# Kernel optimization log

Hardware: AMD Instinct MI355X
Metric: run time of the kernel (lower is better)

The kernel has to match this reference:

```python
import jax, jax.numpy as jnp
import numpy as np

# Config constants from the module
E = 64    # n_routed_experts
K = 6     # num_experts_per_tok
D = 128   # hidden_size
M = 80    # moe_intermediate_size
MS = 160  # shared expert intermediate = moe_intermediate_size * n_shared_experts
B, S = 64, 256

def _init_w(k, shape, fan_in):
    # kaiming_uniform(a=sqrt(5)) used by nn.Linear / MoEGate: bound = 1/sqrt(fan_in)
    bound = 1.0 / np.sqrt(fan_in)
    return jax.random.uniform(k, shape, jnp.float32, -bound, bound)

def setup_inputs() -> dict:
    key = jax.random.key(0)
    ks = jax.random.split(key, 8)
    return {
        "hidden_states": jax.random.normal(ks[0], (B, S, D), jnp.float32),
        "gate_w": _init_w(ks[1], (E, D), D),        # MoEGate.linear.weight [E, gating_dim]
        "wg": _init_w(ks[2], (E, D, M), D),          # stacked expert gate_proj (transposed)
        "wu": _init_w(ks[3], (E, D, M), D),          # stacked expert up_proj
        "wd": _init_w(ks[4], (E, M, D), M),          # stacked expert down_proj
        "swg": _init_w(ks[5], (D, MS), D),           # shared expert gate_proj
        "swu": _init_w(ks[6], (D, MS), D),           # shared expert up_proj
        "swd": _init_w(ks[7], (MS, D), MS),          # shared expert down_proj
    }

def reference(hidden_states, gate_w, wg, wu, wd, swg, swu, swd):
    orig_shape = hidden_states.shape
    x = hidden_states.reshape(-1, D)                       # [T, D] flat tokens
    T = x.shape[0]
    # --- MoEGate ('all_agent' mode): softmax scoring + top-k + renorm ---
    scores = jax.nn.softmax(x @ gate_w.T, axis=-1)          # [T, E]
    topk_w, topk_idx = jax.lax.top_k(scores, K)             # [T, K]
    topk_w = topk_w / (jnp.sum(topk_w, axis=-1, keepdims=True) + 1e-20)
    # Scatter top-k weights into dense per-expert combine weights [T, E]
    cw = jnp.zeros_like(scores).at[jnp.arange(T)[:, None], topk_idx].add(topk_w)
    # --- Routed experts: SiLU-gated MLP per expert, combined by cw ---
    g = jax.nn.silu(jnp.einsum('td,edm->tem', x, wg)) * jnp.einsum('td,edm->tem', x, wu)
    y = jnp.einsum('tem,emd,te->td', g, wd, cw)             # down-proj + weighted combine
    # --- Shared experts ---
    shared = (jax.nn.silu(x @ swg) * (x @ swu)) @ swd       # [T, D]
    return (y + shared).reshape(orig_shape)
```

## Files before the change

kernel.cpp:

```cpp
#include <hip/hip_runtime.h>
#include <hip/hip_bf16.h>
#include <math.h>


typedef unsigned short ushort_t;
typedef __attribute__((ext_vector_type(8))) short bf16x8;
typedef __attribute__((ext_vector_type(4))) float f32x4;

#define EALL  66

#define OFF_TOPKI 16384
#define OFF_WORK  409600
#define OFF_TOPKW 802816
#define OFF_PERM  1196032
#define OFF_PERMW 1589248
#define OFF_POS2  1982464
#define OFF_YPERM 2375680
#define OFF_YSH   27541504
#define OFF_WGT   31735808
#define OFF_WUT   33087488
#define OFF_WDP   34439168
#define OFF_XB    36061184
#define OFF_HIST  40255488
#define OFF_BOFF  40321024
#define NEED_FAST 40386560
#define FOFF_YBUF 2375680
#define FOFF_WGT  10764288
#define FOFF_WUT  12115968
#define FOFF_WDP  13467648
#define FOFF_XB   15089664
#define FOFF_HIST 19283968
#define FOFF_BOFF 19349504

__device__ __forceinline__ float bf2f(ushort_t u) {
    unsigned int x = ((unsigned int)u) << 16;
    float f; __builtin_memcpy(&f, &x, 4); return f;
}
__device__ __forceinline__ ushort_t f2bf(float f) {
    unsigned int x; __builtin_memcpy(&x, &f, 4);
    unsigned int r = (x + 0x7fffu + ((x >> 16) & 1u)) >> 16;
    return (ushort_t)r;
}
__device__ __forceinline__ float ldin(const void* p, int i, int f32m) {
    return f32m ? ((const float*)p)[i] : bf2f(((const ushort_t*)p)[i]);
}
__device__ __forceinline__ int detect_f32m(const ushort_t* gw) {
    int lane = threadIdx.x & 63;
    int cnt = 0;
    #pragma unroll
    for (int j = 0; j < 4; ++j) {
        ushort_t u = gw[lane * 4 + j];
        if (((u >> 7) & 0xFF) >= 0x7C) cnt++;
    }
    #pragma unroll
    for (int off = 32; off; off >>= 1) cnt += __shfl_xor(cnt, off);
    return (cnt >= 8) ? 1 : 0;
}
__device__ __forceinline__ void gl16(void* l, const void* g) {
    __builtin_amdgcn_global_load_lds(
        (const __attribute__((address_space(1))) void*)g,
        (__attribute__((address_space(3))) void*)l, 16, 0, 0);
}

__global__ __launch_bounds__(1024) void k_pg(const void* x, const void* gw,
        const void* wg, const void* wu, const void* wd,
        const void* swg, const void* swu, const void* swd,
        ushort_t* wgT, ushort_t* wuT, ushort_t* wdP,
        ushort_t* xB, int* topk_i, float* topk_w, int* histPart) {
    __shared__ __align__(16) char smem[41984];
    int tid = threadIdx.x, bid = blockIdx.x;
    int f32m = detect_f32m((const ushort_t*)gw);

    if (bid < 3 * EALL) {
        float* lds = (float*)smem;
        int mat = bid / EALL, e = bid % EALL;
        if (mat < 2) {
            const void* src  = (mat == 0) ? wg  : wu;
            const void* ssrc = (mat == 0) ? swg : swu;
            for (int i = tid; i < 10240; i += 1024) {
                int d = i / 80, m = i % 80;
                float v = (e < 64) ? ldin(src, e * 10240 + i, f32m)
                                   : ldin(ssrc, d * 160 + (e - 64) * 80 + m, f32m);
                lds[d * 81 + m] = v;
            }
            __syncthreads();
            ushort_t* dst = ((mat == 0) ? wgT : wuT) + e * 10240;
            for (int o = tid; o < 10240; o += 1024) {
                int m = o >> 7, d = o & 127;
                dst[o] = f2bf(lds[d * 81 + m]);
            }
        } else {
            for (int i = tid; i < 10240; i += 1024) {
                float v = (e < 64) ? ldin(wd, e * 10240 + i, f32m)
                                   : ldin(swd, (e - 64) * 10240 + i, f32m);
                int m = i >> 7, d = i & 127;
                lds[m * 129 + d] = v;
            }
            __syncthreads();
            ushort_t* dst = wdP + e * 12288;
            for (int o = tid; o < 12288; o += 1024) {
                int d = o / 96, m = o % 96;
                dst[o] = (m < 80) ? f2bf(lds[m * 129 + d]) : (ushort_t)0;
            }
        }
        return;
    }

    float* gwl  = (float*)smem;
    float (*xl)[128] = (float(*)[128])(smem + 33280);
    int*   histL = (int*)(smem + 41472);
    int b = bid - 3 * EALL;
    for (int i = tid; i < 8192; i += 1024)
        gwl[(i >> 7) * 130 + (i & 127)] = ldin(gw, i, f32m);
    if (tid < 64) histL[tid] = 0;
    __syncthreads();
    int wv = tid >> 6, lane = tid & 63;
    for (int q = 0; q < 4; ++q) {
        int t = b * 64 + wv * 4 + q;
        float xv0, xv1;
        if (f32m) {
            float2 v = ((const float2*)((const float*)x + t * 128))[lane];
            xv0 = v.x; xv1 = v.y;
        } else {
            unsigned int pr = *(const unsigned int*)((const ushort_t*)x + t * 128 + lane * 2);
            xv0 = bf2f((ushort_t)(pr & 0xffffu));
            xv1 = bf2f((ushort_t)(pr >> 16));
        }
        float2 xw; xw.x = xv0; xw.y = xv1;
        *(float2*)&xl[wv][lane * 2] = xw;
        unsigned int packed = (unsigned int)f2bf(xv0) | ((unsigned int)f2bf(xv1) << 16);
        *(unsigned int*)(xB + t * 128 + lane * 2) = packed;
        float acc = 0.f;
        #pragma unroll
        for (int d2 = 0; d2 < 64; ++d2) {
            float2 xv = *(const float2*)&xl[wv][d2 * 2];
            float2 gv = *(const float2*)&gwl[lane * 130 + d2 * 2];
            acc = fmaf(xv.x, gv.x, acc);
            acc = fmaf(xv.y, gv.y, acc);
        }
        float mx = acc;
        #pragma unroll
        for (int off = 32; off; off >>= 1) mx = fmaxf(mx, __shfl_xor(mx, off));
        float p = expf(acc - mx);
        float sm = p;
        #pragma unroll
        for (int off = 32; off; off >>= 1) sm += __shfl_xor(sm, off);
        float sc = p / sm;
        float cur = sc;
        float wk6[6]; int ik[6];
        #pragma unroll
        for (int k = 0; k < 6; ++k) {
            float bv = cur; int bi = lane;
            #pragma unroll
            for (int off = 1; off < 64; off <<= 1) {
                float ov = __shfl_xor(bv, off); int oi = __shfl_xor(bi, off);
                if (ov > bv || (ov == bv && oi < bi)) { bv = ov; bi = oi; }
            }
            wk6[k] = bv; ik[k] = bi;
            if (lane == bi) cur = -INFINITY;
        }
        if (lane == 0) {
            float den = wk6[0] + wk6[1] + wk6[2] + wk6[3] + wk6[4] + wk6[5] + 1e-20f;
            #pragma unroll
            for (int k = 0; k < 6; ++k) {
                topk_i[t * 6 + k] = ik[k];
                topk_w[t * 6 + k] = wk6[k] / den;
                atomicAdd(&histL[ik[k]], 1);
            }
        }
    }
    __syncthreads();
    if (tid < 64) histPart[tid * 256 + b] = histL[tid];
}

__global__ __launch_bounds__(256) void k_scan(int* Wi, const int* histPart,
        int* boffG, int* wk) {
    __shared__ int hl[16384];
    __shared__ int cntL[64], exclL[64], chxL[65];
    int tid = threadIdx.x, lane = tid & 63, wv = tid >> 6;
    for (int j = tid; j < 16384; j += 256) hl[j] = histPart[j];
    __syncthreads();
    for (int ei = 0; ei < 16; ++ei) {
        int e = wv * 16 + ei;
        int carry = 0;
        for (int r = 0; r < 4; ++r) {
            int v = hl[e * 256 + r * 64 + lane];
            int incl = v;
            #pragma unroll
            for (int off = 1; off < 64; off <<= 1) {
                int ts = __shfl_up(incl, off);
                if (lane >= off) incl += ts;
            }
            hl[e * 256 + r * 64 + lane] = carry + incl - v;
            carry += __shfl(incl, 63);
        }
        if (lane == 0) cntL[e] = carry;
    }
    __syncthreads();
    if (tid == 0) {
        int s = 0, cs = 0;
        for (int e = 0; e < 64; ++e) {
            exclL[e] = s; s += cntL[e];
            chxL[e] = cs; cs += (cntL[e] + 127) >> 7;
        }
        chxL[64] = cs;
        Wi[128] = s;
        Wi[193] = cs + 256;
    }
    __syncthreads();
    if (tid < 64) { Wi[tid] = cntL[tid]; Wi[64 + tid] = exclL[tid]; }
    for (int j = tid; j < 16384; j += 256) boffG[j] = hl[j] + exclL[j >> 8];
    wk[tid] = (64 << 16) | tid;
    if (tid < 64) {
        int e = tid, nc = (cntL[e] + 127) >> 7, bb = chxL[e];
        for (int c = 0; c < nc; ++c) wk[256 + bb + c] = (e << 16) | c;
    }
}

__global__ __launch_bounds__(256) void k_scatter(const int* topk_i, const float* topk_w,
        const int* boffG, int* perm, float* permw, int* pos2) {
    __shared__ int lcur[64];
    int tid = threadIdx.x, b = blockIdx.x;
    if (tid < 64) lcur[tid] = boffG[tid * 256 + b];
    __syncthreads();
    for (int i = tid; i < 384; i += 256) {
        int g = b * 384 + i;
        int e = topk_i[g];
        float w = topk_w[g];
        int p = atomicAdd(&lcur[e], 1);
        perm[p]  = b * 64 + i / 6;
        permw[p] = w;
        pos2[g]  = p;
    }
}

template<int FAST>
__global__ __launch_bounds__(256) void k_expert(const ushort_t* x, const ushort_t* wgT,
        const ushort_t* wuT, const ushort_t* wdP, const int* Wi, const int* wk,
        const int* perm, const float* permw, ushort_t* yperm, ushort_t* ysh, float* ybuf) {
    __shared__ __align__(16) char hl[32768];
    __shared__ __align__(16) char bufA[20480];
    __shared__ __align__(16) char bufB[20480];

    if (blockIdx.x >= Wi[193]) return;
    int entry = wk[blockIdx.x];
    int e = entry >> 16, c = entry & 0xffff;
    int tid = threadIdx.x, lid = tid & 63, wv = tid >> 6;
    int kg  = (lid >> 4) * 16;
    int kq8 = (lid >> 4) * 8;

    if (e < 64) {
        int n = Wi[e], base = Wi[64 + e];
        int nrows = n - c * 128; if (nrows > 128) nrows = 128;

        {
            const ushort_t* gS = wgT + e * 10240;
            const ushort_t* uS = wuT + e * 10240;
            #pragma unroll
            for (int i = 0; i < 5; ++i) {
                int s = wv * 320 + i * 64 + lid;
                int row = s >> 4, sc = (s & 15) ^ (row & 7);
                gl16(bufA + wv * 5120 + i * 1024, gS + row * 128 + sc * 8);
                gl16(bufB + wv * 5120 + i * 1024, uS + row * 128 + sc * 8);
            }
        }
        bf16x8 a[2][4];
        #pragma unroll
        for (int tr = 0; tr < 2; ++tr) {
            int arow = wv * 32 + tr * 16 + (lid & 15);
            int r = (arow < nrows) ? arow : (nrows - 1);
            int t = perm[base + c * 128 + r];
            #pragma unroll
            for (int k = 0; k < 4; ++k)
                a[tr][k] = *(const bf16x8*)(x + t * 128 + k * 32 + kq8);
        }
        __syncthreads();

        #pragma unroll
        for (int mi = 0; mi < 5; ++mi) {
            int brow = mi * 16 + (lid & 15);
            int bro = brow * 256, bsw = (brow & 7) << 4;
            f32x4 ag[2], au[2];
            #pragma unroll
            for (int tr = 0; tr < 2; ++tr) {
                ag[tr] = (f32x4){0.f, 0.f, 0.f, 0.f};
                au[tr] = (f32x4){0.f, 0.f, 0.f, 0.f};
            }
            #pragma unroll
            for (int k = 0; k < 4; ++k) {
                int bo = bro + (((k * 64) + kg) ^ bsw);
                bf16x8 bg = *(const bf16x8*)(bufA + bo);
                bf16x8 bu = *(const bf16x8*)(bufB + bo);
                #pragma unroll
                for (int tr = 0; tr < 2; ++tr) {
                    ag[tr] = __builtin_amdgcn_mfma_f32_16x16x32_bf16(a[tr][k], bg, ag[tr], 0, 0, 0);
                    au[tr] = __builtin_amdgcn_mfma_f32_16x16x32_bf16(a[tr][k], bu, au[tr], 0, 0, 0);
                }
            }
            #pragma unroll
            for (int tr = 0; tr < 2; ++tr) {
                #pragma unroll
                for (int rg = 0; rg < 4; ++rg) {
                    float g = ag[tr][rg], uu2 = au[tr][rg];
                    float h = (g / (1.f + __expf(-g))) * uu2;
                    int row = wv * 32 + tr * 16 + (lid >> 4) * 4 + rg;
                    int cb = (mi * 16 + (lid & 15)) * 2;
                    *(ushort_t*)(hl + row * 256 + (cb ^ ((row & 7) << 4))) = f2bf(h);
                }
            }
        }
        {
            int r = wv * 32 + (lid >> 1), ch = 10 + (lid & 1);
            uint4 z = {0u, 0u, 0u, 0u};
            *(uint4*)(hl + r * 256 + ((ch * 16) ^ ((r & 7) << 4))) = z;
        }
        __syncthreads();

        {
            const ushort_t* dS = wdP + e * 12288;
            #pragma unroll
            for (int i = 0; i < 4; ++i) {
                int s = wv * 256 + i * 64 + lid;
                int r = s >> 4, sc = (s & 15) ^ (r & 7);
                int off = (sc < 12) ? sc * 8 : 0;
                gl16(bufA + wv * 4096 + i * 1024, dS + r * 96 + off);
                gl16(bufB + wv * 4096 + i * 1024, dS + (64 + r) * 96 + off);
            }
        }
        __syncthreads();

        f32x4 acc[8][2];
        #pragma unroll
        for (int dt = 0; dt < 8; ++dt) {
            acc[dt][0] = (f32x4){0.f, 0.f, 0.f, 0.f};
            acc[dt][1] = (f32x4){0.f, 0.f, 0.f, 0.f};
        }
        #pragma unroll
        for (int dt = 0; dt < 8; ++dt) {
            int r = (dt & 3) * 16 + (lid & 15);
            const char* wb = (dt < 4) ? bufA : bufB;
            bf16x8 ad[3];
            #pragma unroll
            for (int k = 0; k < 3; ++k)
                ad[k] = *(const bf16x8*)(wb + r * 256 + (((k * 64) + kg) ^ ((r & 7) << 4)));
            #pragma unroll
            for (int tf = 0; tf < 2; ++tf) {
                int brow = wv * 32 + tf * 16 + (lid & 15);
                f32x4 cc = acc[dt][tf];
                #pragma unroll
                for (int k = 0; k < 3; ++k) {
                    bf16x8 b = *(const bf16x8*)(hl + brow * 256 + (((k * 64) + kg) ^ ((brow & 7) << 4)));
                    cc = __builtin_amdgcn_mfma_f32_16x16x32_bf16(ad[k], b, cc, 0, 0, 0);
                }
                acc[dt][tf] = cc;
            }
        }

        #pragma unroll
        for (int tf = 0; tf < 2; ++tf) {
            int rloc = wv * 32 + tf * 16 + (lid & 15);
            int rc = (rloc < nrows) ? rloc : (nrows - 1);
            float w = FAST ? permw[base + c * 128 + rc] : 0.f;
            #pragma unroll
            for (int dt = 0; dt < 8; ++dt) {
                if (FAST) {
                    int cb = (dt * 16 + (lid >> 4) * 4) * 2;
                    ushort_t o[4];
                    #pragma unroll
                    for (int rg = 0; rg < 4; ++rg) o[rg] = f2bf(acc[dt][tf][rg] * w);
                    *(uint2*)(hl + rloc * 256 + (cb ^ ((rloc & 7) << 4))) = *(const uint2*)o;
                } else {
                    if (rloc < nrows) {
                        int t = perm[base + c * 128 + rloc];
                        float w2 = permw[base + c * 128 + rloc];
                        int d0 = dt * 16 + (lid >> 4) * 4;
                        #pragma unroll
                        for (int rg = 0; rg < 4; ++rg)
                            atomicAdd(&ybuf[t * 128 + d0 + rg], acc[dt][tf][rg] * w2);
                    }
                }
            }
        }
        if (FAST) {
            #pragma unroll
            for (int ps = 0; ps < 8; ++ps) {
                int row = wv * 32 + ps * 4 + (lid >> 4);
                int cb = (lid & 15) * 16;
                uint4 v = *(const uint4*)(hl + row * 256 + (cb ^ ((row & 7) << 4)));
                if (row < nrows)
                    *(uint4*)(yperm + (size_t)(base + c * 128 + row) * 128 + (lid & 15) * 8) = v;
            }
        }
    } else {
        bf16x8 a1[4];
        int arow = wv * 16 + (lid & 15);
        int t0 = c * 64 + arow;
        #pragma unroll
        for (int k = 0; k < 4; ++k)
            a1[k] = *(const bf16x8*)(x + t0 * 128 + k * 32 + kq8);

        f32x4 acc[8];
        #pragma unroll
        for (int dt = 0; dt < 8; ++dt) acc[dt] = (f32x4){0.f, 0.f, 0.f, 0.f};

        for (int sub = 0; sub < 2; ++sub) {
            int ee = 64 + sub;
            {
                const ushort_t* gS = wgT + ee * 10240;
                const ushort_t* uS = wuT + ee * 10240;
                #pragma unroll
                for (int i = 0; i < 5; ++i) {
                    int s = wv * 320 + i * 64 + lid;
                    int row = s >> 4, sc = (s & 15) ^ (row & 7);
                    gl16(bufA + wv * 5120 + i * 1024, gS + row * 128 + sc * 8);
                    gl16(bufB + wv * 5120 + i * 1024, uS + row * 128 + sc * 8);
                }
            }
            __syncthreads();
            #pragma unroll
            for (int mi = 0; mi < 5; ++mi) {
                int brow = mi * 16 + (lid & 15);
                int bro = brow * 256, bsw = (brow & 7) << 4;
                f32x4 ag = {0.f, 0.f, 0.f, 0.f};
                f32x4 au = {0.f, 0.f, 0.f, 0.f};
                #pragma unroll
                for (int k = 0; k < 4; ++k) {
                    int bo = bro + (((k * 64) + kg) ^ bsw);
                    bf16x8 bg = *(const bf16x8*)(bufA + bo);
                    bf16x8 bu = *(const bf16x8*)(bufB + bo);
                    ag = __builtin_amdgcn_mfma_f32_16x16x32_bf16(a1[k], bg, ag, 0, 0, 0);
                    au = __builtin_amdgcn_mfma_f32_16x16x32_bf16(a1[k], bu, au, 0, 0, 0);
                }
                #pragma unroll
                for (int rg = 0; rg < 4; ++rg) {
                    float g = ag[rg], uu2 = au[rg];
                    float h = (g / (1.f + __expf(-g))) * uu2;
                    int row = wv * 16 + (lid >> 4) * 4 + rg;
                    int cb = (mi * 16 + (lid & 15)) * 2;
                    *(ushort_t*)(hl + row * 256 + (cb ^ ((row & 7) << 4))) = f2bf(h);
                }
            }
            if (sub == 0 && lid < 32) {
                int r = wv * 16 + (lid >> 1), ch = 10 + (lid & 1);
                uint4 z = {0u, 0u, 0u, 0u};
                *(uint4*)(hl + r * 256 + ((ch * 16) ^ ((r & 7) << 4))) = z;
            }
            __syncthreads();
            {
                const ushort_t* dS = wdP + ee * 12288;
                #pragma unroll
                for (int i = 0; i < 4; ++i) {
                    int s = wv * 256 + i * 64 + lid;
                    int r = s >> 4, sc = (s & 15) ^ (r & 7);
                    int off = (sc < 12) ? sc * 8 : 0;
                    gl16(bufA + wv * 4096 + i * 1024, dS + r * 96 + off);
                    gl16(bufB + wv * 4096 + i * 1024, dS + (64 + r) * 96 + off);
                }
            }
            __syncthreads();
            int brow = wv * 16 + (lid & 15);
            #pragma unroll
            for (int dt = 0; dt < 8; ++dt) {
                int r = (dt & 3) * 16 + (lid & 15);
                const char* wb = (dt < 4) ? bufA : bufB;
                bf16x8 ad[3];
                #pragma unroll
                for (int k = 0; k < 3; ++k)
                    ad[k] = *(const bf16x8*)(wb + r * 256 + (((k * 64) + kg) ^ ((r & 7) << 4)));
                f32x4 cc = acc[dt];
                #pragma unroll
                for (int k = 0; k < 3; ++k) {
                    bf16x8 b = *(const bf16x8*)(hl + brow * 256 + (((k * 64) + kg) ^ ((brow & 7) << 4)));
                    cc = __builtin_amdgcn_mfma_f32_16x16x32_bf16(ad[k], b, cc, 0, 0, 0);
                }
                acc[dt] = cc;
            }
            __syncthreads();
        }

        int rloc = wv * 16 + (lid & 15);
        if (FAST) {
            #pragma unroll
            for (int dt = 0; dt < 8; ++dt) {
                int cb = (dt * 16 + (lid >> 4) * 4) * 2;
                ushort_t o[4];
                #pragma unroll
                for (int rg = 0; rg < 4; ++rg) o[rg] = f2bf(acc[dt][rg]);
                *(uint2*)(hl + rloc * 256 + (cb ^ ((rloc & 7) << 4))) = *(const uint2*)o;
            }
            #pragma unroll
            for (int ps = 0; ps < 4; ++ps) {
                int row = wv * 16 + ps * 4 + (lid >> 4);
                int cb = (lid & 15) * 16;
                uint4 v = *(const uint4*)(hl + row * 256 + (cb ^ ((row & 7) << 4)));
                *(uint4*)(ysh + (size_t)(c * 64 + row) * 128 + (lid & 15) * 8) = v;
            }
        } else {
            int t = c * 64 + rloc;
            #pragma unroll
            for (int dt = 0; dt < 8; ++dt) {
                int d0 = dt * 16 + (lid >> 4) * 4;
                #pragma unroll
                for (int rg = 0; rg < 4; ++rg)
                    atomicAdd(&ybuf[t * 128 + d0 + rg], acc[dt][rg]);
            }
        }
    }
}

__global__ __launch_bounds__(256) void k_final_gather(const ushort_t* yperm,
        const ushort_t* ysh, const int* pos2, void* out, const ushort_t* gwDet) {
    int idx = blockIdx.x * 256 + threadIdx.x;
    int t = idx >> 4, cg = (idx & 15) * 8;
    int f32m = detect_f32m(gwDet);
    float acc[8];
    {
        uint4 v = *(const uint4*)(ysh + (size_t)t * 128 + cg);
        const ushort_t* u = (const ushort_t*)&v;
        #pragma unroll
        for (int j = 0; j < 8; ++j) acc[j] = bf2f(u[j]);
    }
    const int* pp = pos2 + t * 6;
    #pragma unroll
    for (int k = 0; k < 6; ++k) {
        int p = pp[k];
        uint4 v = *(const uint4*)(yperm + (size_t)p * 128 + cg);
        const ushort_t* u = (const ushort_t*)&v;
        #pragma unroll
        for (int j = 0; j < 8; ++j) acc[j] += bf2f(u[j]);
    }
    if (f32m) {
        float4 o0 = {acc[0], acc[1], acc[2], acc[3]};
        float4 o1 = {acc[4], acc[5], acc[6], acc[7]};
        float* op = (float*)out + (size_t)t * 128 + cg;
        *(float4*)op = o0; *(float4*)(op + 4) = o1;
    } else {
        ushort_t o[8];
        #pragma unroll
        for (int j = 0; j < 8; ++j) o[j] = f2bf(acc[j]);
        *(uint4*)((ushort_t*)out + (size_t)t * 128 + cg) = *(const uint4*)o;
    }
}

__global__ __launch_bounds__(256) void k_final_ybuf(const float* ybuf, void* out,
        const ushort_t* gwDet) {
    int i = blockIdx.x * 256 + threadIdx.x;
    int f32m = detect_f32m(gwDet);
    float4 v = ((const float4*)ybuf)[i];
    if (f32m) {
        ((float4*)out)[i] = v;
    } else {
        ushort4 o;
        o.x = f2bf(v.x); o.y = f2bf(v.y); o.z = f2bf(v.z); o.w = f2bf(v.w);
        ((ushort4*)out)[i] = o;
    }
}

extern "C" void kernel_launch(void* const* d_in, const int* in_sizes, int n_in,
                              void* d_out, int out_size, void* d_ws, size_t ws_size,
                              hipStream_t stream) {
    (void)in_sizes; (void)n_in; (void)out_size;
    const void* x   = d_in[0];
    const void* gw  = d_in[1];
    const void* wg  = d_in[2];
    const void* wu  = d_in[3];
    const void* wd  = d_in[4];
    const void* swg = d_in[5];
    const void* swu = d_in[6];
    const void* swd = d_in[7];

    char* ws = (char*)d_ws;
    int fast = (ws_size >= (size_t)NEED_FAST) ? 1 : 0;

    int*      Wi     = (int*)d_ws;
    int*      topk_i = (int*)(ws + OFF_TOPKI);
    int*      wklist = (int*)(ws + OFF_WORK);
    float*    topk_w = (float*)(ws + OFF_TOPKW);
    int*      perm   = (int*)(ws + OFF_PERM);
    float*    permw  = (float*)(ws + OFF_PERMW);
    int*      pos2   = (int*)(ws + OFF_POS2);

    ushort_t* yperm = (ushort_t*)(ws + OFF_YPERM);
    ushort_t* ysh   = (ushort_t*)(ws + OFF_YSH);
    float*    ybuf  = (float*)(ws + FOFF_YBUF);
    ushort_t* wgT   = (ushort_t*)(ws + (fast ? OFF_WGT  : FOFF_WGT));
    ushort_t* wuT   = (ushort_t*)(ws + (fast ? OFF_WUT  : FOFF_WUT));
    ushort_t* wdP   = (ushort_t*)(ws + (fast ? OFF_WDP  : FOFF_WDP));
    ushort_t* xB    = (ushort_t*)(ws + (fast ? OFF_XB   : FOFF_XB));
    int*      histP = (int*)(ws + (fast ? OFF_HIST : FOFF_HIST));
    int*      boffG = (int*)(ws + (fast ? OFF_BOFF : FOFF_BOFF));

    if (!fast) hipMemsetAsync(ybuf, 0, 16384 * 128 * 4, stream);

    k_pg<<<3 * EALL + 256, 1024, 0, stream>>>(x, gw, wg, wu, wd, swg, swu, swd,
                                              wgT, wuT, wdP, xB, topk_i, topk_w, histP);
    k_scan<<<1, 256, 0, stream>>>(Wi, histP, boffG, wklist);
    k_scatter<<<256, 256, 0, stream>>>(topk_i, topk_w, boffG, perm, permw, pos2);
    if (fast) {
        k_expert<1><<<1088, 256, 0, stream>>>(xB, wgT, wuT, wdP, Wi, wklist, perm, permw, yperm, ysh, ybuf);
        k_final_gather<<<1024, 256, 0, stream>>>(yperm, ysh, pos2, d_out, (const ushort_t*)gw);
    } else {
        k_expert<0><<<1088, 256, 0, stream>>>(xB, wgT, wuT, wdP, Wi, wklist, perm, permw, yperm, ysh, ybuf);
        k_final_ybuf<<<2048, 256, 0, stream>>>(ybuf, d_out, (const ushort_t*)gw);
    }
}
```

Measured before the change: 92.81 us.

## Unify shared-expert path into routed tile code with 128-token tiles

Shared-expert blocks now process 128 tokens per block instead of 64, which halves the shared-expert work items from 256 to 128 and removes the separate code path by reusing the routed 2-tile-per-wave loop with a sub-expert loop. The down-projection B fragments from the activation tile are also hoisted into registers once per sub-expert rather than reloaded for each output tile. This cuts block count and redundant weight loads, at the cost of higher register pressure and fewer parallel blocks for the shared experts.

```diff
diff --git a/kernel.cpp b/kernel.cpp
--- a/kernel.cpp
+++ b/kernel.cpp
@@ -205,15 +205,15 @@
         }
         chxL[64] = cs;
         Wi[128] = s;
-        Wi[193] = cs + 256;
+        Wi[193] = cs + 128;
     }
     __syncthreads();
     if (tid < 64) { Wi[tid] = cntL[tid]; Wi[64 + tid] = exclL[tid]; }
     for (int j = tid; j < 16384; j += 256) boffG[j] = hl[j] + exclL[j >> 8];
-    wk[tid] = (64 << 16) | tid;
+    if (tid < 128) wk[tid] = (64 << 16) | tid;
     if (tid < 64) {
         int e = tid, nc = (cntL[e] + 127) >> 7, bb = chxL[e];
-        for (int c = 0; c < nc; ++c) wk[256 + bb + c] = (e << 16) | c;
+        for (int c = 0; c < nc; ++c) wk[128 + bb + c] = (e << 16) | c;
     }
 }
 
@@ -249,13 +249,44 @@
     int kg  = (lid >> 4) * 16;
     int kq8 = (lid >> 4) * 8;
 
+    int nrows = 128, base = 0;
+    int nsub = 1;
     if (e < 64) {
-        int n = Wi[e], base = Wi[64 + e];
-        int nrows = n - c * 128; if (nrows > 128) nrows = 128;
+        int n = Wi[e]; base = Wi[64 + e];
+        nrows = n - c * 128; if (nrows > 128) nrows = 128;
+    } else {
+        nsub = 2;
+    }
+
+    bf16x8 a[2][4];
+    #pragma unroll
+    for (int tr = 0; tr < 2; ++tr) {
+        int arow = wv * 32 + tr * 16 + (lid & 15);
+        int t;
+        if (e < 64) {
+            int r = (arow < nrows) ? arow : (nrows - 1);
+            t = perm[base + c * 128 + r];
+        } else {
+            t = c * 128 + arow;
+        }
+        #pragma unroll
+        for (int k = 0; k < 4; ++k)
+            a[tr][k] = *(const bf16x8*)(x + t * 128 + k * 32 + kq8);
+    }
+
+    f32x4 acc[8][2];
+    #pragma unroll
+    for (int dt = 0; dt < 8; ++dt) {
+        acc[dt][0] = (f32x4){0.f, 0.f, 0.f, 0.f};
+        acc[dt][1] = (f32x4){0.f, 0.f, 0.f, 0.f};
+    }
+
+    for (int sub = 0; sub < nsub; ++sub) {
+        int ee = (e < 64) ? e : (64 + sub);
 
         {
-            const ushort_t* gS = wgT + e * 10240;
-            const ushort_t* uS = wuT + e * 10240;
+            const ushort_t* gS = wgT + ee * 10240;
+            const ushort_t* uS = wuT + ee * 10240;
             #pragma unroll
             for (int i = 0; i < 5; ++i) {
                 int s = wv * 320 + i * 64 + lid;
@@ -263,16 +294,6 @@
                 gl16(bufA + wv * 5120 + i * 1024, gS + row * 128 + sc * 8);
                 gl16(bufB + wv * 5120 + i * 1024, uS + row * 128 + sc * 8);
             }
-        }
-        bf16x8 a[2][4];
-        #pragma unroll
-        for (int tr = 0; tr < 2; ++tr) {
-            int arow = wv * 32 + tr * 16 + (lid & 15);
-            int r = (arow < nrows) ? arow : (nrows - 1);
-            int t = perm[base + c * 128 + r];
-            #pragma unroll
-            for (int k = 0; k < 4; ++k)
-                a[tr][k] = *(const bf16x8*)(x + t * 128 + k * 32 + kq8);
         }
         __syncthreads();
 
@@ -309,7 +330,7 @@
                 }
             }
         }
-        {
+        if (sub == 0) {
             int r = wv * 32 + (lid >> 1), ch = 10 + (lid & 1);
             uint4 z = {0u, 0u, 0u, 0u};
             *(uint4*)(hl + r * 256 + ((ch * 16) ^ ((r & 7) << 4))) = z;
@@ -317,7 +338,7 @@
         __syncthreads();
 
         {
-            const ushort_t* dS = wdP + e * 12288;
+            const ushort_t* dS = wdP + ee * 12288;
             #pragma unroll
             for (int i = 0; i < 4; ++i) {
                 int s = wv * 256 + i * 64 + lid;
@@ -329,11 +350,13 @@
         }
         __syncthreads();
 
-        f32x4 acc[8][2];
-        #pragma unroll
-        for (int dt = 0; dt < 8; ++dt) {
-            acc[dt][0] = (f32x4){0.f, 0.f, 0.f, 0.f};
-            acc[dt][1] = (f32x4){0.f, 0.f, 0.f, 0.f};
+        bf16x8 bfr[2][3];
+        #pragma unroll
+        for (int tf = 0; tf < 2; ++tf) {
+            int brow = wv * 32 + tf * 16 + (lid & 15);
+            #pragma unroll
+            for (int k = 0; k < 3; ++k)
+                bfr[tf][k] = *(const bf16x8*)(hl + brow * 256 + (((k * 64) + kg) ^ ((brow & 7) << 4)));
         }
         #pragma unroll
         for (int dt = 0; dt < 8; ++dt) {
@@ -345,164 +368,55 @@
                 ad[k] = *(const bf16x8*)(wb + r * 256 + (((k * 64) + kg) ^ ((r & 7) << 4)));
             #pragma unroll
             for (int tf = 0; tf < 2; ++tf) {
-                int brow = wv * 32 + tf * 16 + (lid & 15);
                 f32x4 cc = acc[dt][tf];
                 #pragma unroll
-                for (int k = 0; k < 3; ++k) {
-                    bf16x8 b = *(const bf16x8*)(hl + brow * 256 + (((k * 64) + kg) ^ ((brow & 7) << 4)));
-                    cc = __builtin_amdgcn_mfma_f32_16x16x32_bf16(ad[k], b, cc, 0, 0, 0);
-                }
+                for (int k = 0; k < 3; ++k)
+                    cc = __builtin_amdgcn_mfma_f32_16x16x32_bf16(ad[k], bfr[tf][k], cc, 0, 0, 0);
                 acc[dt][tf] = cc;
             }
         }
-
-        #pragma unroll
-        for (int tf = 0; tf < 2; ++tf) {
-            int rloc = wv * 32 + tf * 16 + (lid & 15);
-            int rc = (rloc < nrows) ? rloc : (nrows - 1);
-            float w = FAST ? permw[base + c * 128 + rc] : 0.f;
-            #pragma unroll
-            for (int dt = 0; dt < 8; ++dt) {
-                if (FAST) {
-                    int cb = (dt * 16 + (lid >> 4) * 4) * 2;
-                    ushort_t o[4];
-                    #pragma unroll
-                    for (int rg = 0; rg < 4; ++rg) o[rg] = f2bf(acc[dt][tf][rg] * w);
-                    *(uint2*)(hl + rloc * 256 + (cb ^ ((rloc & 7) << 4))) = *(const uint2*)o;
-                } else {
-                    if (rloc < nrows) {
-                        int t = perm[base + c * 128 + rloc];
-                        float w2 = permw[base + c * 128 + rloc];
-                        int d0 = dt * 16 + (lid >> 4) * 4;
-                        #pragma unroll
-                        for (int rg = 0; rg < 4; ++rg)
-                            atomicAdd(&ybuf[t * 128 + d0 + rg], acc[dt][tf][rg] * w2);
-                    }
-                }
-            }
-        }
-        if (FAST) {
-            #pragma unroll
-            for (int ps = 0; ps < 8; ++ps) {
-                int row = wv * 32 + ps * 4 + (lid >> 4);
-                int cb = (lid & 15) * 16;
-                uint4 v = *(const uint4*)(hl + row * 256 + (cb ^ ((row & 7) << 4)));
-                if (row < nrows)
-                    *(uint4*)(yperm + (size_t)(base + c * 128 + row) * 128 + (lid & 15) * 8) = v;
-            }
-        }
-    } else {
-        bf16x8 a1[4];
-        int arow = wv * 16 + (lid & 15);
-        int t0 = c * 64 + arow;
-        #pragma unroll
-        for (int k = 0; k < 4; ++k)
-            a1[k] = *(const bf16x8*)(x + t0 * 128 + k * 32 + kq8);
-
-        f32x4 acc[8];
-        #pragma unroll
-        for (int dt = 0; dt < 8; ++dt) acc[dt] = (f32x4){0.f, 0.f, 0.f, 0.f};
-
-        for (int sub = 0; sub < 2; ++sub) {
-            int ee = 64 + sub;
-            {
-                const ushort_t* gS = wgT + ee * 10240;
-                const ushort_t* uS = wuT + ee * 10240;
-                #pragma unroll
-                for (int i = 0; i < 5; ++i) {
-                    int s = wv * 320 + i * 64 + lid;
-                    int row = s >> 4, sc = (s & 15) ^ (row & 7);
-                    gl16(bufA + wv * 5120 + i * 1024, gS + row * 128 + sc * 8);
-                    gl16(bufB + wv * 5120 + i * 1024, uS + row * 128 + sc * 8);
-                }
-            }
-            __syncthreads();
-            #pragma unroll
-            for (int mi = 0; mi < 5; ++mi) {
-                int brow = mi * 16 + (lid & 15);
-                int bro = brow * 256, bsw = (brow & 7) << 4;
-                f32x4 ag = {0.f, 0.f, 0.f, 0.f};
-                f32x4 au = {0.f, 0.f, 0.f, 0.f};
-                #pragma unroll
-                for (int k = 0; k < 4; ++k) {
-                    int bo = bro + (((k * 64) + kg) ^ bsw);
-                    bf16x8 bg = *(const bf16x8*)(bufA + bo);
-                    bf16x8 bu = *(const bf16x8*)(bufB + bo);
-                    ag = __builtin_amdgcn_mfma_f32_16x16x32_bf16(a1[k], bg, ag, 0, 0, 0);
-                    au = __builtin_amdgcn_mfma_f32_16x16x32_bf16(a1[k], bu, au, 0, 0, 0);
-                }
-                #pragma unroll
-                for (int rg = 0; rg < 4; ++rg) {
-                    float g = ag[rg], uu2 = au[rg];
-                    float h = (g / (1.f + __expf(-g))) * uu2;
-                    int row = wv * 16 + (lid >> 4) * 4 + rg;
-                    int cb = (mi * 16 + (lid & 15)) * 2;
-                    *(ushort_t*)(hl + row * 256 + (cb ^ ((row & 7) << 4))) = f2bf(h);
-                }
-            }
-            if (sub == 0 && lid < 32) {
-                int r = wv * 16 + (lid >> 1), ch = 10 + (lid & 1);
-                uint4 z = {0u, 0u, 0u, 0u};
-                *(uint4*)(hl + r * 256 + ((ch * 16) ^ ((r & 7) << 4))) = z;
-            }
-            __syncthreads();
-            {
-                const ushort_t* dS = wdP + ee * 12288;
-                #pragma unroll
-                for (int i = 0; i < 4; ++i) {
-                    int s = wv * 256 + i * 64 + lid;
-                    int r = s >> 4, sc = (s & 15) ^ (r & 7);
-                    int off = (sc < 12) ? sc * 8 : 0;
-                    gl16(bufA + wv * 4096 + i * 1024, dS + r * 96 + off);
-                    gl16(bufB + wv * 4096 + i * 1024, dS + (64 + r) * 96 + off);
-                }
-            }
-            __syncthreads();
-            int brow = wv * 16 + (lid & 15);
-            #pragma unroll
-            for (int dt = 0; dt < 8; ++dt) {
-                int r = (dt & 3) * 16 + (lid & 15);
-                const char* wb = (dt < 4) ? bufA : bufB;
-                bf16x8 ad[3];
-                #pragma unroll
-                for (int k = 0; k < 3; ++k)
-                    ad[k] = *(const bf16x8*)(wb + r * 256 + (((k * 64) + kg) ^ ((r & 7) << 4)));
-                f32x4 cc = acc[dt];
-                #pragma unroll
-                for (int k = 0; k < 3; ++k) {
-                    bf16x8 b = *(const bf16x8*)(hl + brow * 256 + (((k * 64) + kg) ^ ((brow & 7) << 4)));
-                    cc = __builtin_amdgcn_mfma_f32_16x16x32_bf16(ad[k], b, cc, 0, 0, 0);
-                }
-                acc[dt] = cc;
-            }
-            __syncthreads();
-        }
-
-        int rloc = wv * 16 + (lid & 15);
-        if (FAST) {
-            #pragma unroll
-            for (int dt = 0; dt < 8; ++dt) {
+        if (sub + 1 < nsub) __syncthreads();
+    }
+
+    #pragma unroll
+    for (int tf = 0; tf < 2; ++tf) {
+        int rloc = wv * 32 + tf * 16 + (lid & 15);
+        int rc = (rloc < nrows) ? rloc : (nrows - 1);
+        float w;
+        if (e < 64) w = FAST ? permw[base + c * 128 + rc] : 0.f;
+        else        w = 1.0f;
+        #pragma unroll
+        for (int dt = 0; dt < 8; ++dt) {
+            if (FAST) {
                 int cb = (dt * 16 + (lid >> 4) * 4) * 2;
                 ushort_t o[4];
                 #pragma unroll
-                for (int rg = 0; rg < 4; ++rg) o[rg] = f2bf(acc[dt][rg]);
+                for (int rg = 0; rg < 4; ++rg) o[rg] = f2bf(acc[dt][tf][rg] * w);
                 *(uint2*)(hl + rloc * 256 + (cb ^ ((rloc & 7) << 4))) = *(const uint2*)o;
-            }
-            #pragma unroll
-            for (int ps = 0; ps < 4; ++ps) {
-                int row = wv * 16 + ps * 4 + (lid >> 4);
-                int cb = (lid & 15) * 16;
-                uint4 v = *(const uint4*)(hl + row * 256 + (cb ^ ((row & 7) << 4)));
-                *(uint4*)(ysh + (size_t)(c * 64 + row) * 128 + (lid & 15) * 8) = v;
-            }
-        } else {
-            int t = c * 64 + rloc;
-            #pragma unroll
-            for (int dt = 0; dt < 8; ++dt) {
-                int d0 = dt * 16 + (lid >> 4) * 4;
-                #pragma unroll
-                for (int rg = 0; rg < 4; ++rg)
-                    atomicAdd(&ybuf[t * 128 + d0 + rg], acc[dt][rg]);
+            } else {
+                if (rloc < nrows) {
+                    int t; float w2;
+                    if (e < 64) { t = perm[base + c * 128 + rloc]; w2 = permw[base + c * 128 + rloc]; }
+                    else        { t = c * 128 + rloc; w2 = 1.0f; }
+                    int d0 = dt * 16 + (lid >> 4) * 4;
+                    #pragma unroll
+                    for (int rg = 0; rg < 4; ++rg)
+                        atomicAdd(&ybuf[t * 128 + d0 + rg], acc[dt][tf][rg] * w2);
+                }
+            }
+        }
+    }
+    if (FAST) {
+        #pragma unroll
+        for (int ps = 0; ps < 8; ++ps) {
+            int row = wv * 32 + ps * 4 + (lid >> 4);
+            int cb = (lid & 15) * 16;
+            uint4 v = *(const uint4*)(hl + row * 256 + (cb ^ ((row & 7) << 4)));
+            if (row < nrows) {
+                ushort_t* dst = (e < 64)
+                    ? (yperm + (size_t)(base + c * 128 + row) * 128)
+                    : (ysh   + (size_t)(c * 128 + row) * 128);
+                *(uint4*)(dst + (lid & 15) * 8) = v;
             }
         }
     }
```

Result: slower. 103.4 us (+11.4%).
